# Performance work log

Hardware: AMD Instinct MI355X
Metric: run time of the kernel (lower is better)

The kernel has to match this reference:

```python
import jax, jax.numpy as jnp
import numpy as np

B, C_IN, C_OUT, H, W, W_DIM, K = 4, 64, 64, 512, 512, 512, 3
LRELU_SLOPE = 0.2
ACT_GAIN = np.sqrt(2.0).astype(np.float32)  # lrelu def_gain
CONV_CLAMP = 256.0


def setup_inputs() -> dict:
    key = jax.random.key(0)
    ks = jax.random.split(key, 5)
    return {
        "x": jax.random.normal(ks[0], (B, C_IN, H, W), dtype=jnp.float32),
        "ws": jax.random.normal(ks[1], (B, W_DIM), dtype=jnp.float32),
        "noise": jax.random.normal(ks[2], (B, 1, H, W), dtype=jnp.float32),
        "affine_weight": jax.random.normal(ks[3], (C_IN, W_DIM), dtype=jnp.float32),
        "affine_bias": jnp.ones((C_IN,), dtype=jnp.float32),
        "conv_weight": jax.random.normal(ks[4], (C_OUT, C_IN, K, K), dtype=jnp.float32),
        "bias": jnp.zeros((C_OUT,), dtype=jnp.float32),
    }


def reference(x, ws, noise, affine_weight, affine_bias, conv_weight, bias):
    b, c_in, h, w_sp = x.shape
    c_out, _, kh, kw = conv_weight.shape
    w_dim = ws.shape[1]

    # Affine (FullyConnectedLayer with equalized LR: weight_gain = 1/sqrt(w_dim), bias_init=1)
    styles = ws @ (affine_weight.T * np.float32(1.0 / np.sqrt(w_dim))) + affine_bias  # [b, c_in]

    # Modulate per-sample weights: w = weight[None] * styles
    wmod = conv_weight[None] * styles[:, None, :, None, None]  # [b, c_out, c_in, kh, kw]

    # Demodulation coefficients
    demod = jax.lax.rsqrt(jnp.sum(jnp.square(wmod), axis=(2, 3, 4)) + 1e-8)  # [b, c_out]
    wmod = wmod * demod[:, :, None, None, None]

    # Fused grouped conv: groups = batch (conv2d_resample, up=down=1, flip_weight=True -> correlation)
    xg = x.reshape(1, b * c_in, h, w_sp)
    wg = wmod.reshape(b * c_out, c_in, kh, kw)
    pad = kh // 2
    y = jax.lax.conv_general_dilated(
        xg, wg, window_strides=(1, 1), padding=[(pad, pad), (pad, pad)],
        dimension_numbers=("NCHW", "OIHW", "NCHW"), feature_group_count=b)
    y = y.reshape(b, c_out, h, w_sp)

    # Noise add (broadcast over channels)
    y = y + noise

    # bias_act: bias + lrelu * act_gain, then clamp (conv_clamp * gain, gain=1)
    y = y + bias[None, :, None, None]
    y = jnp.where(y >= 0, y, LRELU_SLOPE * y) * ACT_GAIN
    y = jnp.clip(y, -CONV_CLAMP, CONV_CLAMP)
    return y
```

## Files before the change

### kernel.cpp

```cpp
#include <hip/hip_runtime.h>
#include <math.h>

#define HH 512
#define WW 512
#define HW (HH * WW)
#define PW 514
#define PPIX (PW * PW)

#define A_U 36864
#define B_U 22016
#define LDS_BYTES ((A_U + 2 * B_U) * 2)

typedef short bf16x8 __attribute__((ext_vector_type(8)));
typedef float f32x4  __attribute__((ext_vector_type(4)));
typedef float f32x16 __attribute__((ext_vector_type(16)));

__device__ __forceinline__ ushort f2bf(float f) {
    union { float f; uint u; } c; c.f = f;
    uint u = c.u;
    return (ushort)((u + 0x7fffu + ((u >> 16) & 1u)) >> 16);
}

__device__ __forceinline__ uint cvtpk(float a, float b) {
    uint r;
    asm("v_cvt_pk_bf16_f32 %0, %1, %2" : "=v"(r) : "v"(a), "v"(b));
    return r;
}

__global__ void k_styles(const float* __restrict__ wsv, const float* __restrict__ aw,
                         const float* __restrict__ ab, float* __restrict__ styles) {
    int bid = blockIdx.x;
    int b = bid >> 6, ci = bid & 63;
    int l = threadIdx.x;
    const float* wrow = wsv + b * 512;
    const float* arow = aw + ci * 512;
    float s = 0.f;
    #pragma unroll
    for (int j = 0; j < 8; ++j)
        s += wrow[l + 64 * j] * arow[l + 64 * j];
    #pragma unroll
    for (int off = 32; off; off >>= 1)
        s += __shfl_xor(s, off, 64);
    if (l == 0)
        styles[b * 64 + ci] = s * 0.044194173824159216f + ab[ci];
}

__global__ void k_wmod(const float* __restrict__ cw, const float* __restrict__ styles,
                       ushort* __restrict__ wb) {
    int b = blockIdx.x >> 6, co = blockIdx.x & 63;
    int ci = threadIdx.x;
    float st = styles[b * 64 + ci];
    const float* wp = cw + (co * 64 + ci) * 9;
    float wv[9];
    float ss = 0.f;
    #pragma unroll
    for (int k = 0; k < 9; ++k) { wv[k] = wp[k] * st; ss += wv[k] * wv[k]; }
    #pragma unroll
    for (int off = 32; off; off >>= 1)
        ss += __shfl_xor(ss, off, 64);
    float dm = 1.0f / sqrtf(ss + 1e-8f);
    int cisw = ((((ci >> 3) ^ co) & 7) << 3) | (ci & 7);
    #pragma unroll
    for (int k = 0; k < 9; ++k)
        wb[((size_t)(b * 64 + co) * 9 + k) * 64 + cisw] = f2bf(wv[k] * dm);
}

__global__ __launch_bounds__(256) void k_xpose(
    const float* __restrict__ x, ushort* __restrict__ xp) {
    const int t = threadIdx.x;
    const int bid = blockIdx.x;

    if (bid >= 8192) {
        int id = (bid - 8192) * 256 + t;
        if (id >= 4 * 2052) return;
        int b = id / 2052, r = id % 2052;
        int gyp, gxp;
        if (r < 514)       { gyp = 0;        gxp = r; }
        else if (r < 1028) { gyp = 513;      gxp = r - 514; }
        else if (r < 1540) { gyp = r - 1027; gxp = 0; }
        else               { gyp = r - 1539; gxp = 513; }
        ushort* p = xp + (((size_t)b * PW + gyp) * PW + gxp) * 64;
        uint4 z = make_uint4(0, 0, 0, 0);
        #pragma unroll
        for (int i = 0; i < 8; ++i) *(uint4*)(p + i * 8) = z;
        return;
    }

    __shared__ ushort lt[128 * 68];
    const int gxt = bid & 3;
    const int gy  = (bid >> 2) & 511;
    const int b   = bid >> 11;

    const float* xb = x + (size_t)b * 64 * HW + (size_t)gy * WW + gxt * 128;
    const int ci0 = 8 * (t >> 5);
    const int gxc = t & 31;

    f32x4 v[8];
    #pragma unroll
    for (int j = 0; j < 8; ++j)
        v[j] = *(const f32x4*)(xb + (size_t)(ci0 + j) * HW + gxc * 4);

    #pragma unroll
    for (int p = 0; p < 4; ++p) {
        int px = gxc * 4 + p;
        int rowp = ((px & 3) * 32 + (px >> 2)) * 68;
        #pragma unroll
        for (int cg = 0; cg < 2; ++cg) {
            uint lo = cvtpk(v[4 * cg + 0][p], v[4 * cg + 1][p]);
            uint hi = cvtpk(v[4 * cg + 2][p], v[4 * cg + 3][p]);
            *(uint2*)&lt[rowp + ci0 + 4 * cg] = make_uint2(lo, hi);
        }
    }
    __syncthreads();

    const int px = t >> 1, half = t & 1;
    const int rowp = ((px & 3) * 32 + (px >> 2)) * 68 + half * 32;
    uint4 o0 = *(uint4*)&lt[rowp + 0];
    uint4 o1 = *(uint4*)&lt[rowp + 8];
    uint4 o2 = *(uint4*)&lt[rowp + 16];
    uint4 o3 = *(uint4*)&lt[rowp + 24];
    ushort* dst = xp + (((size_t)b * PW + (gy + 1)) * PW + (gxt * 128 + px + 1)) * 64
                     + half * 32;
    *(uint4*)(dst + 0)  = o0;
    *(uint4*)(dst + 8)  = o1;
    *(uint4*)(dst + 16) = o2;
    *(uint4*)(dst + 24) = o3;
}

__global__ __launch_bounds__(256, 1) void k_conv(
    const ushort* __restrict__ xp,
    const ushort* __restrict__ wb,
    const float* __restrict__ noise,
    const float* __restrict__ bias,
    float* __restrict__ out) {
    extern __shared__ __align__(16) ushort lds[];

    const int t = threadIdx.x;
    const int w = t >> 6;
    const int lane = t & 63;
    const int n5 = lane & 31;
    const int hl = lane >> 5;
    const int blk = blockIdx.x;
    const int b = blk >> 6;
    const int band = blk & 63;
    const int ty = band * 8;

    const ushort* xpb = xp + (size_t)b * PPIX * 64;
    const ushort* wA  = wb + (size_t)b * 64 * 576;

    #pragma unroll
    for (int jj = 0; jj < 18; ++jj) {
        int j = w + jj * 4;
        const ushort* src = wA + j * 512 + lane * 8;
        __builtin_amdgcn_global_load_lds(
            (const __attribute__((address_space(1))) unsigned int*)src,
            (__attribute__((address_space(3))) unsigned int*)&lds[j * 512],
            16, 0, 0);
    }

    int soff[11];
    #pragma unroll
    for (int jj = 0; jj < 11; ++jj) {
        int j = w + jj * 4;
        if (j < 43) {
            int c = j * 64 + lane;
            int c2 = c < 2719 ? c : 2719;
            int cig = c2 & 7;
            int pxl = c2 >> 3;
            int row = pxl / 34;
            int lcol = pxl - row * 34;
            int gsrc = cig ^ (lcol & 7);
            soff[jj] = ((ty + row) * PW + lcol) * 64 + gsrc * 8;
        } else soff[jj] = 0;
    }

    #pragma unroll
    for (int jj = 0; jj < 11; ++jj) {
        int j = w + jj * 4;
        if (j < 43)
            __builtin_amdgcn_global_load_lds(
                (const __attribute__((address_space(1))) unsigned int*)(xpb + soff[jj]),
                (__attribute__((address_space(3))) unsigned int*)&lds[A_U + j * 512],
                16, 0, 0);
    }
    asm volatile("s_waitcnt vmcnt(0)" ::: "memory");
    __syncthreads();

    int aidx[2];
    #pragma unroll
    for (int mt = 0; mt < 2; ++mt)
        aidx[mt] = (mt * 32 + n5) * 576 + ((hl ^ (n5 & 7)) << 3);

    int bidx[2][3];
    const int brow = 2 * w + (n5 >> 4);
    #pragma unroll
    for (int i = 0; i < 2; ++i)
        #pragma unroll
        for (int dx = 0; dx < 3; ++dx) {
            int lcol = i * 16 + (n5 & 15) + dx;
            bidx[i][dx] = (brow * 34 + lcol) * 64 + ((hl ^ (lcol & 7)) << 3);
        }

    const float* nz = noise + (size_t)b * HW;
    const int orow = ty + brow;

    int p = 0;
    for (int it = 0; it < 16; ++it) {
        const int tx = it * 32;

        if (it < 15) {
            #pragma unroll
            for (int jj = 0; jj < 11; ++jj) {
                int j = w + jj * 4;
                if (j < 43)
                    __builtin_amdgcn_global_load_lds(
                        (const __attribute__((address_space(1))) unsigned int*)
                            (xpb + soff[jj] + (tx + 32) * 64),
                        (__attribute__((address_space(3))) unsigned int*)
                            &lds[A_U + (p ^ 1) * B_U + j * 512],
                        16, 0, 0);
            }
        }

        float nv[2];
        #pragma unroll
        for (int i = 0; i < 2; ++i)
            nv[i] = nz[orow * WW + tx + i * 16 + (n5 & 15)];

        const ushort* bufp = &lds[A_U + p * B_U];
        f32x16 acc[2][2];
        #pragma unroll
        for (int mt = 0; mt < 2; ++mt)
            #pragma unroll
            for (int i = 0; i < 2; ++i)
                acc[mt][i] = (f32x16){0.f,0.f,0.f,0.f,0.f,0.f,0.f,0.f,
                                      0.f,0.f,0.f,0.f,0.f,0.f,0.f,0.f};

        #pragma unroll
        for (int dy = 0; dy < 3; ++dy) {
            #pragma unroll
            for (int dx = 0; dx < 3; ++dx) {
                const int off = dy * 3 + dx;
                #pragma unroll
                for (int kb = 0; kb < 4; ++kb) {
                    bf16x8 afr[2], bfr[2];
                    #pragma unroll
                    for (int mt = 0; mt < 2; ++mt)
                        afr[mt] = *(const bf16x8*)
                            &lds[(aidx[mt] + off * 64) ^ (kb << 4)];
                    #pragma unroll
                    for (int i = 0; i < 2; ++i)
                        bfr[i] = *(const bf16x8*)
                            &bufp[(bidx[i][dx] + dy * (34 * 64)) ^ (kb << 4)];
                    #pragma unroll
                    for (int mt = 0; mt < 2; ++mt)
                        #pragma unroll
                        for (int i = 0; i < 2; ++i)
                            acc[mt][i] = __builtin_amdgcn_mfma_f32_32x32x16_bf16(
                                afr[mt], bfr[i], acc[mt][i], 0, 0, 0);
                }
            }
        }

        asm volatile("s_waitcnt vmcnt(0)" ::: "memory");
        __syncthreads();

        #pragma unroll
        for (int mt = 0; mt < 2; ++mt) {
            #pragma unroll
            for (int i = 0; i < 2; ++i) {
                const int ocol = tx + i * 16 + (n5 & 15);
                #pragma unroll
                for (int reg = 0; reg < 16; ++reg) {
                    int co = mt * 32 + (reg & 3) + 8 * (reg >> 2) + 4 * hl;
                    float y = acc[mt][i][reg] + nv[i] + bias[co];
                    y = (y >= 0.f ? y : 0.2f * y) * 1.41421356237f;
                    y = fminf(fmaxf(y, -256.f), 256.f);
                    out[((size_t)(b * 64 + co) * HH + orow) * WW + ocol] = y;
                }
            }
        }
        p ^= 1;
    }
}

extern "C" void kernel_launch(void* const* d_in, const int* in_sizes, int n_in,
                              void* d_out, int out_size, void* d_ws, size_t ws_size,
                              hipStream_t stream) {
    const float* x     = (const float*)d_in[0];
    const float* wsv   = (const float*)d_in[1];
    const float* noise = (const float*)d_in[2];
    const float* aw    = (const float*)d_in[3];
    const float* ab    = (const float*)d_in[4];
    const float* cw    = (const float*)d_in[5];
    const float* bias  = (const float*)d_in[6];
    float* out = (float*)d_out;

    float*  styles = (float*)d_ws;
    ushort* wb16   = (ushort*)((char*)d_ws + 1024);
    ushort* xpad   = (ushort*)((char*)d_ws + (1 << 20));

    hipFuncSetAttribute((const void*)k_conv,
                        hipFuncAttributeMaxDynamicSharedMemorySize, LDS_BYTES);

    k_styles<<<256, 64, 0, stream>>>(wsv, aw, ab, styles);
    k_wmod<<<256, 64, 0, stream>>>(cw, styles, wb16);
    k_xpose<<<8225, 256, 0, stream>>>(x, xpad);
    k_conv<<<256, 256, LDS_BYTES, stream>>>(xpad, wb16, noise, bias, out);
}
```

Measured before the change: 260.5 us.

## Fuse NCHW-to-bf16 transpose and padding into conv kernel staging

Removes the separate transpose/pad kernel and its padded bf16 intermediate buffer. The conv kernel now stages fp32 NCHW tiles into LDS in four channel chunks, converts them to bf16 in the swizzled pixel-major layout, and handles borders with bounds checks. This cuts the extra write and read of the intermediate tensor and one launch. In exchange the single tile buffer is no longer double-buffered, staging is only partly overlapped with the MFMA loop, and several extra barriers are added per iteration.

```diff
diff --git a/kernel.cpp b/kernel.cpp
--- a/kernel.cpp
+++ b/kernel.cpp
@@ -4,12 +4,10 @@
 #define HH 512
 #define WW 512
 #define HW (HH * WW)
-#define PW 514
-#define PPIX (PW * PW)
-
-#define A_U 36864
-#define B_U 22016
-#define LDS_BYTES ((A_U + 2 * B_U) * 2)
+
+#define T_OFF_U 36864
+#define F_OFF_U 58624
+#define LDS_BYTES (F_OFF_U * 2 + 25600)
 
 typedef short bf16x8 __attribute__((ext_vector_type(8)));
 typedef float f32x4  __attribute__((ext_vector_type(4)));
@@ -65,70 +63,8 @@
         wb[((size_t)(b * 64 + co) * 9 + k) * 64 + cisw] = f2bf(wv[k] * dm);
 }
 
-__global__ __launch_bounds__(256) void k_xpose(
-    const float* __restrict__ x, ushort* __restrict__ xp) {
-    const int t = threadIdx.x;
-    const int bid = blockIdx.x;
-
-    if (bid >= 8192) {
-        int id = (bid - 8192) * 256 + t;
-        if (id >= 4 * 2052) return;
-        int b = id / 2052, r = id % 2052;
-        int gyp, gxp;
-        if (r < 514)       { gyp = 0;        gxp = r; }
-        else if (r < 1028) { gyp = 513;      gxp = r - 514; }
-        else if (r < 1540) { gyp = r - 1027; gxp = 0; }
-        else               { gyp = r - 1539; gxp = 513; }
-        ushort* p = xp + (((size_t)b * PW + gyp) * PW + gxp) * 64;
-        uint4 z = make_uint4(0, 0, 0, 0);
-        #pragma unroll
-        for (int i = 0; i < 8; ++i) *(uint4*)(p + i * 8) = z;
-        return;
-    }
-
-    __shared__ ushort lt[128 * 68];
-    const int gxt = bid & 3;
-    const int gy  = (bid >> 2) & 511;
-    const int b   = bid >> 11;
-
-    const float* xb = x + (size_t)b * 64 * HW + (size_t)gy * WW + gxt * 128;
-    const int ci0 = 8 * (t >> 5);
-    const int gxc = t & 31;
-
-    f32x4 v[8];
-    #pragma unroll
-    for (int j = 0; j < 8; ++j)
-        v[j] = *(const f32x4*)(xb + (size_t)(ci0 + j) * HW + gxc * 4);
-
-    #pragma unroll
-    for (int p = 0; p < 4; ++p) {
-        int px = gxc * 4 + p;
-        int rowp = ((px & 3) * 32 + (px >> 2)) * 68;
-        #pragma unroll
-        for (int cg = 0; cg < 2; ++cg) {
-            uint lo = cvtpk(v[4 * cg + 0][p], v[4 * cg + 1][p]);
-            uint hi = cvtpk(v[4 * cg + 2][p], v[4 * cg + 3][p]);
-            *(uint2*)&lt[rowp + ci0 + 4 * cg] = make_uint2(lo, hi);
-        }
-    }
-    __syncthreads();
-
-    const int px = t >> 1, half = t & 1;
-    const int rowp = ((px & 3) * 32 + (px >> 2)) * 68 + half * 32;
-    uint4 o0 = *(uint4*)&lt[rowp + 0];
-    uint4 o1 = *(uint4*)&lt[rowp + 8];
-    uint4 o2 = *(uint4*)&lt[rowp + 16];
-    uint4 o3 = *(uint4*)&lt[rowp + 24];
-    ushort* dst = xp + (((size_t)b * PW + (gy + 1)) * PW + (gxt * 128 + px + 1)) * 64
-                     + half * 32;
-    *(uint4*)(dst + 0)  = o0;
-    *(uint4*)(dst + 8)  = o1;
-    *(uint4*)(dst + 16) = o2;
-    *(uint4*)(dst + 24) = o3;
-}
-
 __global__ __launch_bounds__(256, 1) void k_conv(
-    const ushort* __restrict__ xp,
+    const float* __restrict__ x,
     const ushort* __restrict__ wb,
     const float* __restrict__ noise,
     const float* __restrict__ bias,
@@ -145,8 +81,8 @@
     const int band = blk & 63;
     const int ty = band * 8;
 
-    const ushort* xpb = xp + (size_t)b * PPIX * 64;
-    const ushort* wA  = wb + (size_t)b * 64 * 576;
+    const float* xb = x + (size_t)b * 64 * HW;
+    const ushort* wA = wb + (size_t)b * 64 * 576;
 
     #pragma unroll
     for (int jj = 0; jj < 18; ++jj) {
@@ -158,33 +94,63 @@
             16, 0, 0);
     }
 
-    int soff[11];
-    #pragma unroll
-    for (int jj = 0; jj < 11; ++jj) {
-        int j = w + jj * 4;
-        if (j < 43) {
-            int c = j * 64 + lane;
-            int c2 = c < 2719 ? c : 2719;
-            int cig = c2 & 7;
-            int pxl = c2 >> 3;
-            int row = pxl / 34;
-            int lcol = pxl - row * 34;
-            int gsrc = cig ^ (lcol & 7);
-            soff[jj] = ((ty + row) * PW + lcol) * 64 + gsrc * 8;
-        } else soff[jj] = 0;
+    auto stage_chunk = [&](int cc, int txn) {
+        #pragma unroll
+        for (int kk = 0; kk < 7; ++kk) {
+            int k = w + kk * 4;
+            if (k < 25) {
+                int f = k * 256 + 4 * lane;
+                int ci = f / 400;
+                int rem = f - ci * 400;
+                int row = rem / 40;
+                int col = rem - row * 40;
+                int gy = ty - 1 + row;  gy = gy < 0 ? 0 : (gy > 511 ? 511 : gy);
+                int gx = txn - 4 + col; gx = gx < 0 ? 0 : (gx > 508 ? 508 : gx);
+                const float* src = xb + (size_t)(cc * 16 + ci) * HW + gy * WW + gx;
+                __builtin_amdgcn_global_load_lds(
+                    (const __attribute__((address_space(1))) unsigned int*)src,
+                    (__attribute__((address_space(3))) unsigned int*)
+                        ((unsigned int*)&lds[F_OFF_U] + k * 256),
+                    16, 0, 0);
+            }
+        }
+    };
+
+    auto cvt_chunk = [&](int cc, int txn) {
+        const float* F = (const float*)&lds[F_OFF_U];
+        #pragma unroll
+        for (int q = 0; q < 3; ++q) {
+            int id = t + q * 256;
+            if (id < 680) {
+                int lcol = id % 34;
+                int rem = id / 34;
+                int cs = rem & 1;
+                int row = rem >> 1;
+                int gy = ty - 1 + row;
+                int gxl = txn - 1 + lcol;
+                bool ok = (gy >= 0) && (gy < HH) && (gxl >= 0) && (gxl < WW);
+                int base = (8 * cs) * 400 + row * 40 + (lcol + 3);
+                float v[8];
+                #pragma unroll
+                for (int j = 0; j < 8; ++j)
+                    v[j] = ok ? F[base + j * 400] : 0.f;
+                uint pk[4];
+                #pragma unroll
+                for (int j = 0; j < 4; ++j)
+                    pk[j] = cvtpk(v[2 * j], v[2 * j + 1]);
+                int grp = ((2 * cc + cs) ^ (lcol & 7)) << 3;
+                uint4* dst = (uint4*)&lds[T_OFF_U + (row * 34 + lcol) * 64 + grp];
+                *dst = make_uint4(pk[0], pk[1], pk[2], pk[3]);
+            }
+        }
+    };
+
+    for (int cc = 0; cc < 4; ++cc) {
+        stage_chunk(cc, 0);
+        __syncthreads();
+        cvt_chunk(cc, 0);
+        __syncthreads();
     }
-
-    #pragma unroll
-    for (int jj = 0; jj < 11; ++jj) {
-        int j = w + jj * 4;
-        if (j < 43)
-            __builtin_amdgcn_global_load_lds(
-                (const __attribute__((address_space(1))) unsigned int*)(xpb + soff[jj]),
-                (__attribute__((address_space(3))) unsigned int*)&lds[A_U + j * 512],
-                16, 0, 0);
-    }
-    asm volatile("s_waitcnt vmcnt(0)" ::: "memory");
-    __syncthreads();
 
     int aidx[2];
     #pragma unroll
@@ -204,30 +170,17 @@
     const float* nz = noise + (size_t)b * HW;
     const int orow = ty + brow;
 
-    int p = 0;
     for (int it = 0; it < 16; ++it) {
         const int tx = it * 32;
 
-        if (it < 15) {
-            #pragma unroll
-            for (int jj = 0; jj < 11; ++jj) {
-                int j = w + jj * 4;
-                if (j < 43)
-                    __builtin_amdgcn_global_load_lds(
-                        (const __attribute__((address_space(1))) unsigned int*)
-                            (xpb + soff[jj] + (tx + 32) * 64),
-                        (__attribute__((address_space(3))) unsigned int*)
-                            &lds[A_U + (p ^ 1) * B_U + j * 512],
-                        16, 0, 0);
-            }
-        }
-
         float nv[2];
         #pragma unroll
         for (int i = 0; i < 2; ++i)
             nv[i] = nz[orow * WW + tx + i * 16 + (n5 & 15)];
 
-        const ushort* bufp = &lds[A_U + p * B_U];
+        if (it < 15) stage_chunk(0, tx + 32);
+
+        const ushort* bufp = &lds[T_OFF_U];
         f32x16 acc[2][2];
         #pragma unroll
         for (int mt = 0; mt < 2; ++mt)
@@ -262,8 +215,14 @@
             }
         }
 
-        asm volatile("s_waitcnt vmcnt(0)" ::: "memory");
-        __syncthreads();
+        if (it < 15) {
+            for (int cc = 0; cc < 4; ++cc) {
+                __syncthreads();
+                cvt_chunk(cc, tx + 32);
+                __syncthreads();
+                if (cc < 3) stage_chunk(cc + 1, tx + 32);
+            }
+        }
 
         #pragma unroll
         for (int mt = 0; mt < 2; ++mt) {
@@ -280,7 +239,6 @@
                 }
             }
         }
-        p ^= 1;
     }
 }
 
@@ -298,13 +256,11 @@
 
     float*  styles = (float*)d_ws;
     ushort* wb16   = (ushort*)((char*)d_ws + 1024);
-    ushort* xpad   = (ushort*)((char*)d_ws + (1 << 20));
 
     hipFuncSetAttribute((const void*)k_conv,
                         hipFuncAttributeMaxDynamicSharedMemorySize, LDS_BYTES);
 
     k_styles<<<256, 64, 0, stream>>>(wsv, aw, ab, styles);
     k_wmod<<<256, 64, 0, stream>>>(cw, styles, wb16);
-    k_xpose<<<8225, 256, 0, stream>>>(x, xpad);
-    k_conv<<<256, 256, LDS_BYTES, stream>>>(xpad, wb16, noise, bias, out);
-}
+    k_conv<<<256, 256, LDS_BYTES, stream>>>(x, wb16, noise, bias, out);
+}
```

Result: slower. 275.0 us (+5.6%).
